# Kernel optimization log

Measured on AMD Instinct MI355X. Metric: run time of the kernel, lower is better.

## Reference

```python
import jax, jax.numpy as jnp
import numpy as np

B, L, H, N = 8, 8192, 128, 32  # batch, seq_len, d_model, d_state//2 (complex)


def setup_inputs() -> dict:
    key = jax.random.key(0)
    ks = jax.random.split(key, 13)
    x = jax.random.normal(ks[0], (B, L, 2), dtype=jnp.float32)
    enc_w = jax.random.normal(ks[1], (2, H), dtype=jnp.float32) * (1.0 / np.sqrt(2.0))
    enc_b = jax.random.normal(ks[2], (H,), dtype=jnp.float32) * 0.01
    # S4D init: dt log-uniform in [1e-3, 1e-1], A = -0.5 + i*pi*n (S4D-Lin)
    u01 = jax.random.uniform(ks[3], (H,), dtype=jnp.float32)
    log_dt = u01 * (np.log(0.1) - np.log(0.001)) + np.log(0.001)
    log_A_real = jnp.full((H, N), np.log(0.5), dtype=jnp.float32)
    A_imag = jnp.broadcast_to(np.pi * jnp.arange(N, dtype=jnp.float32), (H, N)).copy()
    C_re = jax.random.normal(ks[4], (H, N), dtype=jnp.float32) * (0.5 ** 0.5)
    C_im = jax.random.normal(ks[5], (H, N), dtype=jnp.float32) * (0.5 ** 0.5)
    D = jax.random.normal(ks[6], (H,), dtype=jnp.float32)
    out_w = jax.random.normal(ks[7], (2 * H, H), dtype=jnp.float32) * (1.0 / np.sqrt(H))
    out_b = jax.random.normal(ks[8], (2 * H,), dtype=jnp.float32) * 0.01
    dec_w = jax.random.normal(ks[9], (H, 1), dtype=jnp.float32) * (1.0 / np.sqrt(H))
    dec_b = jax.random.normal(ks[10], (1,), dtype=jnp.float32) * 0.01
    return {"x": x, "enc_w": enc_w, "enc_b": enc_b, "log_dt": log_dt,
            "log_A_real": log_A_real, "A_imag": A_imag, "C_re": C_re,
            "C_im": C_im, "D": D, "out_w": out_w, "out_b": out_b,
            "dec_w": dec_w, "dec_b": dec_b}


def reference(x, enc_w, enc_b, log_dt, log_A_real, A_imag, C_re, C_im, D,
              out_w, out_b, dec_w, dec_b):
    # Encoder (B,L,2) -> (B,L,H), then transpose to channels-first (B,H,L)
    u = jnp.einsum('blc,ch->blh', x, enc_w) + enc_b
    u = jnp.swapaxes(u, -1, -2)  # (B,H,L)
    Lx = u.shape[-1]

    # --- S4D kernel (zero-order-hold discretization, diagonal A) ---
    dt = jnp.exp(log_dt)                      # (H,)
    A = -jnp.exp(log_A_real) + 1j * A_imag    # (H,N) complex
    C = C_re + 1j * C_im                      # (H,N)
    dtA = dt[:, None] * A                     # (H,N)
    K_coef = C * (jnp.exp(dtA) - 1.0) / A     # (H,N)
    # Vandermonde: exp(dtA * l), l = 0..L-1  -> (H,N,L)
    vand = jnp.exp(dtA[:, :, None] * jnp.arange(Lx, dtype=jnp.float32))
    K = 2.0 * jnp.einsum('hn,hnl->hl', K_coef, vand).real  # (H,L)

    # --- causal convolution via FFT (length 2L avoids circular wrap) ---
    n = 2 * Lx
    y = jnp.fft.irfft(jnp.fft.rfft(u, n) * jnp.fft.rfft(K, n), n)[..., :Lx]
    y = y + D[:, None] * u                    # skip connection

    # GELU -> pointwise GLU output projection (Conv1d(H, 2H, 1) + GLU)
    y = jax.nn.gelu(y)
    z = jnp.einsum('bhl,gh->bgl', y, out_w) + out_b[None, :, None]  # (B,2H,L)
    a, g = jnp.split(z, 2, axis=1)
    y = a * jax.nn.sigmoid(g)                 # (B,H,L)

    # Mean-pool over sequence, decode to scalar: (B,1)
    pooled = jnp.mean(y, axis=-1)             # (B,H)
    return pooled @ dec_w + dec_b
```

## Files before the change

### kernel.cpp

```cpp
#include <hip/hip_runtime.h>
#include <math.h>

#define B_ 8
#define L_ 8192
#define H_ 128
#define N_ 32
#define C_ 128
#define T_ 64


typedef _Float16 half8 __attribute__((ext_vector_type(8)));
typedef __attribute__((ext_vector_type(4))) float f32x4;

__device__ __forceinline__ float gelu_tanh(float y) {
    float t = 0.7978845608028654f * fmaf(0.044715f, y * y * y, y);
    float e = __expf(2.f * t);
    float th = 1.f - __fdividef(2.f, e + 1.f);
    return 0.5f * y * (1.f + th);
}
__device__ __forceinline__ unsigned short f2h(float f) {
    _Float16 h = (_Float16)f;
    return *(unsigned short*)&h;
}
__device__ __forceinline__ float h2f(unsigned short u) {
    return (float)(*(const _Float16*)&u);
}
__device__ __forceinline__ unsigned int pk2(float a, float b) {
    return (unsigned)f2h(a) | ((unsigned)f2h(b) << 16);
}

__global__ __launch_bounds__(256, 4) void k_s4d(
    const float* __restrict__ x, const float* __restrict__ enc_w,
    const float* __restrict__ enc_b, const float* __restrict__ log_dt,
    const float* __restrict__ log_A_real, const float* __restrict__ A_imag,
    const float* __restrict__ C_re, const float* __restrict__ C_im,
    const float* __restrict__ Dp, const float* __restrict__ out_w,
    unsigned short* __restrict__ Wh, unsigned short* __restrict__ gy)
{
    const int bh = blockIdx.x;
    const int b = bh >> 7, h = bh & (H_ - 1);
    const int tid = threadIdx.x;
    const int lane = tid & 63, wq = tid >> 6;
    const int mrow = lane & 15, quad = lane >> 4;

    __shared__ unsigned short Ut[C_][72];
    __shared__ __align__(16) char scratch[18432];
    __shared__ float2 wTpow[7][N_];
    __shared__ float2 coefs[N_];
    __shared__ float2 ArAi[N_];
    __shared__ float  Kd[64];
    unsigned short* E16 = (unsigned short*)scratch;
    float2*         Sx  = (float2*)scratch;
    unsigned short* St  = (unsigned short*)scratch;

    const float dt = expf(log_dt[h]);
    const float Dh = Dp[h];

    if (tid < N_) {
        int n = tid;
        float Ar = -expf(log_A_real[h * N_ + n]);
        float Ai = A_imag[h * N_ + n];
        ArAi[n] = make_float2(Ar, Ai);
        float ar = dt * Ar, ai = dt * Ai;
        float er = expf(ar);
        float wr = er * cosf(ai), wi = er * sinf(ai);
        float inv = 1.f / (Ar * Ar + Ai * Ai);
        float numr = wr - 1.f, numi = wi;
        float qr = (numr * Ar + numi * Ai) * inv;
        float qi = (numi * Ar - numr * Ai) * inv;
        coefs[n] = make_float2(C_re[h * N_ + n] * qr - C_im[h * N_ + n] * qi,
                               C_re[h * N_ + n] * qi + C_im[h * N_ + n] * qr);
        float arT = dt * Ar * (float)T_, aiT = dt * Ai * (float)T_;
        float erT = expf(arT);
        float pr = erT * cosf(aiT), pi = erT * sinf(aiT);
#pragma unroll
        for (int k = 0; k < 7; ++k) {
            wTpow[k][n] = make_float2(pr, pi);
            float nr = pr * pr - pi * pi;
            pi = 2.f * pr * pi; pr = nr;
        }
    }

    if (b == 0) {
        int g = 2 * h + (tid >> 7), j = tid & 127;
        Wh[g * 128 + j] = f2h(out_w[g * 128 + j]);
    }

    const float ew0 = enc_w[h], ew1 = enc_w[H_ + h], eb = enc_b[h];
    {
        int c = tid >> 1, j0 = (tid & 1) * 32;
        const float4* xp = (const float4*)((const float2*)x + (size_t)b * L_
                                           + c * 64 + j0);
#pragma unroll
        for (int i = 0; i < 16; ++i) {
            float4 xv = xp[i];
            float u0 = fmaf(xv.x, ew0, fmaf(xv.y, ew1, eb));
            float u1 = fmaf(xv.z, ew0, fmaf(xv.w, ew1, eb));
            *(unsigned int*)&Ut[c][j0 + 2 * i] = pk2(u0, u1);
        }
    }
    __syncthreads();

    {
        int t = tid >> 2, q = tid & 3;
        float s = 0.f;
        float ft = (float)t;
#pragma unroll
        for (int k = 0; k < 8; ++k) {
            int n = q * 8 + k;
            float2 cf = coefs[n]; float2 aa = ArAi[n];
            float er = __expf(dt * aa.x * ft);
            float sn, cs; __sincosf(dt * aa.y * ft, &sn, &cs);
            s = fmaf(cf.x, er * cs, s);
            s = fmaf(-cf.y, er * sn, s);
        }
        ((float*)&Ut[t][64])[q] = s;
    }

    {
        f32x4 acc[8];
#pragma unroll
        for (int nt = 0; nt < 8; ++nt) acc[nt] = (f32x4){0.f, 0.f, 0.f, 0.f};
        const int m = wq * 16 + mrow;
        const float2 aa = ArAi[m & 31];
        const float dAr = dt * aa.x, dAi = dt * aa.y;
        const bool isIm = (m >= 32);
#pragma unroll
        for (int ks = 0; ks < 2; ++ks) {
            int k0 = ks * 32 + quad * 8;
            half8 af;
#pragma unroll
            for (int i = 0; i < 8; ++i) {
                float d = (float)(63 - (k0 + i));
                float er = __expf(dAr * d);
                float sn, cs; __sincosf(dAi * d, &sn, &cs);
                af[i] = (_Float16)(isIm ? er * sn : er * cs);
            }
#pragma unroll
            for (int nt = 0; nt < 8; ++nt) {
                half8 bf = *(const half8*)&Ut[nt * 16 + mrow][k0];
                acc[nt] = __builtin_amdgcn_mfma_f32_16x16x32_f16(
                    af, bf, acc[nt], 0, 0, 0);
            }
        }
        const int m0 = wq * 16 + quad * 4;
#pragma unroll
        for (int nt = 0; nt < 8; ++nt) {
            int cc = nt * 16 + mrow;
            unsigned long long w =
                (unsigned long long)pk2(acc[nt][0], acc[nt][1]) |
                ((unsigned long long)pk2(acc[nt][2], acc[nt][3]) << 32);
            *(unsigned long long*)&E16[cc * 72 + m0] = w;
        }
    }
    __syncthreads();

    if (tid < 64) {
        const float* kp = (const float*)&Ut[tid][64];
        Kd[tid] = 2.f * (kp[0] + kp[1] + kp[2] + kp[3])
                  + ((tid == 0) ? Dh : 0.f);
    }

    float zr[16], zi[16];
    const int cHalf = wq & 1, nHalf = wq >> 1;
    const int n0 = nHalf * 16;
    const int c = cHalf * 64 + lane;
    {
        half8 ha = *(const half8*)(E16 + c * 72 + n0);
        half8 hb = *(const half8*)(E16 + c * 72 + n0 + 8);
        half8 hc = *(const half8*)(E16 + c * 72 + 32 + n0);
        half8 hd = *(const half8*)(E16 + c * 72 + 32 + n0 + 8);
#pragma unroll
        for (int j = 0; j < 8; ++j) {
            zr[j] = (float)ha[j];  zr[8 + j] = (float)hb[j];
            zi[j] = (float)hc[j];  zi[8 + j] = (float)hd[j];
        }
    }
    __syncthreads();
#pragma unroll
    for (int k = 0; k < 6; ++k) {
        int s = 1 << k;
        float mask = (lane >= s) ? 1.f : 0.f;
#pragma unroll
        for (int j = 0; j < 16; ++j) {
            float2 q = wTpow[k][n0 + j];
            float vr = __shfl_up(zr[j], s, 64);
            float vi = __shfl_up(zi[j], s, 64);
            float adr = fmaf(q.x, vr, -(q.y * vi));
            float adi = fmaf(q.x, vi, q.y * vr);
            zr[j] = fmaf(mask, adr, zr[j]);
            zi[j] = fmaf(mask, adi, zi[j]);
        }
    }
    if (cHalf == 0) {
#pragma unroll
        for (int j = 0; j < 16; ++j)
            Sx[(n0 + j) * 64 + lane] = make_float2(zr[j], zi[j]);
    }
    __syncthreads();
    if (cHalf == 1) {
#pragma unroll
        for (int j = 0; j < 16; ++j) {
            float2 q = wTpow[6][n0 + j];
            float2 v = Sx[(n0 + j) * 64 + lane];
            zr[j] = fmaf(q.x, v.x, fmaf(-q.y, v.y, zr[j]));
            zi[j] = fmaf(q.x, v.y, fmaf(q.y, v.x, zi[j]));
        }
    }
    {
        bool l0 = (lane == 0);
#pragma unroll
        for (int j = 0; j < 16; ++j) {
            float2 bv = Sx[(n0 + j) * 64 + 63];
            float br = (cHalf == 1) ? bv.x : 0.f;
            float bi = (cHalf == 1) ? bv.y : 0.f;
            float tr = __shfl_up(zr[j], 1, 64);
            float ti = __shfl_up(zi[j], 1, 64);
            zr[j] = l0 ? br : tr;
            zi[j] = l0 ? bi : ti;
        }
    }
    __syncthreads();
    {
        uint4 w0, w1;
        w0.x = pk2(zr[0], zr[1]);   w0.y = pk2(zr[2], zr[3]);
        w0.z = pk2(zr[4], zr[5]);   w0.w = pk2(zr[6], zr[7]);
        w1.x = pk2(zr[8], zr[9]);   w1.y = pk2(zr[10], zr[11]);
        w1.z = pk2(zr[12], zr[13]); w1.w = pk2(zr[14], zr[15]);
        *(uint4*)&St[c * 72 + n0] = w0;
        *(uint4*)&St[c * 72 + n0 + 8] = w1;
        w0.x = pk2(zi[0], zi[1]);   w0.y = pk2(zi[2], zi[3]);
        w0.z = pk2(zi[4], zi[5]);   w0.w = pk2(zi[6], zi[7]);
        w1.x = pk2(zi[8], zi[9]);   w1.y = pk2(zi[10], zi[11]);
        w1.z = pk2(zi[12], zi[13]); w1.w = pk2(zi[14], zi[15]);
        *(uint4*)&St[c * 72 + 32 + n0] = w0;
        *(uint4*)&St[c * 72 + 32 + n0 + 8] = w1;
    }
    __syncthreads();

    {
        f32x4 acc[8];
#pragma unroll
        for (int nt = 0; nt < 8; ++nt) acc[nt] = (f32x4){0.f, 0.f, 0.f, 0.f};
        const int t = wq * 16 + mrow;
#pragma unroll
        for (int ks = 0; ks < 2; ++ks) {
            int k0 = ks * 32 + quad * 8;
            half8 af;
#pragma unroll
            for (int i = 0; i < 8; ++i) {
                int j = k0 + i;
                af[i] = (_Float16)((t >= j) ? Kd[t - j] : 0.f);
            }
#pragma unroll
            for (int nt = 0; nt < 8; ++nt) {
                half8 bf = *(const half8*)&Ut[nt * 16 + mrow][k0];
                acc[nt] = __builtin_amdgcn_mfma_f32_16x16x32_f16(
                    bf, af, acc[nt], 0, 0, 0);
            }
        }
        half8 afP0, afP1;
        {
            float tp1 = (float)(t + 1);
#pragma unroll
            for (int i = 0; i < 8; ++i) {
                int n = quad * 8 + i;
                float2 cf = coefs[n]; float2 aa = ArAi[n];
                float er = __expf(dt * aa.x * tp1);
                float sn, cs; __sincosf(dt * aa.y * tp1, &sn, &cs);
                float wr = er * cs, wi = er * sn;
                afP0[i] = (_Float16)( 2.f * (cf.x * wr - cf.y * wi));
                afP1[i] = (_Float16)(-2.f * (cf.x * wi + cf.y * wr));
            }
        }
#pragma unroll
        for (int ks = 0; ks < 2; ++ks) {
            int k0 = ks * 32 + quad * 8;
            half8 af = ks ? afP1 : afP0;
#pragma unroll
            for (int nt = 0; nt < 8; ++nt) {
                half8 bf = *(const half8*)&St[(nt * 16 + mrow) * 72 + k0];
                acc[nt] = __builtin_amdgcn_mfma_f32_16x16x32_f16(
                    bf, af, acc[nt], 0, 0, 0);
            }
        }
        unsigned short* gyr = gy + (size_t)bh * L_ + (size_t)t * 128;
#pragma unroll
        for (int nt = 0; nt < 8; ++nt) {
            float g0 = gelu_tanh(acc[nt][0]);
            float g1 = gelu_tanh(acc[nt][1]);
            float g2 = gelu_tanh(acc[nt][2]);
            float g3 = gelu_tanh(acc[nt][3]);
            unsigned long long w =
                (unsigned long long)pk2(g0, g1) |
                ((unsigned long long)pk2(g2, g3) << 32);
            *(unsigned long long*)&gyr[nt * 16 + quad * 4] = w;
        }
    }
}

__global__ __launch_bounds__(256, 4) void k_mix(
    const unsigned short* __restrict__ Wh, const unsigned short* __restrict__ gy,
    const float* __restrict__ out_b, const float* __restrict__ dec_w,
    float* __restrict__ part)
{
    __shared__ unsigned short Bt[64 * 128];
    __shared__ float red[4];

    const int blk = blockIdx.x;
    const int b = blk >> 7;
    const int t = (blk >> 1) & 63, ch = blk & 1;
    const int tid = threadIdx.x;
    const int wq = tid >> 6, lane = tid & 63;

    const unsigned short* gsrc = gy + (size_t)(b * H_) * L_ + t * 128 + ch * 64;
#pragma unroll
    for (int it = 0; it < 4; ++it) {
        int idx = it * 256 + tid;
        int h = idx >> 3, v0 = (idx & 7) * 8;
        uint4 q = *(const uint4*)(gsrc + (size_t)h * L_ + v0);
        const int sw = (((h >> 3) ^ (idx & 7)) << 3) | (h & 7);
        Bt[(v0 + 0) * 128 + sw] = (unsigned short)(q.x & 0xFFFF);
        Bt[(v0 + 1) * 128 + sw] = (unsigned short)(q.x >> 16);
        Bt[(v0 + 2) * 128 + sw] = (unsigned short)(q.y & 0xFFFF);
        Bt[(v0 + 3) * 128 + sw] = (unsigned short)(q.y >> 16);
        Bt[(v0 + 4) * 128 + sw] = (unsigned short)(q.z & 0xFFFF);
        Bt[(v0 + 5) * 128 + sw] = (unsigned short)(q.z >> 16);
        Bt[(v0 + 6) * 128 + sw] = (unsigned short)(q.w & 0xFFFF);
        Bt[(v0 + 7) * 128 + sw] = (unsigned short)(q.w >> 16);
    }
    __syncthreads();

    const int ga = wq * 32;
    const int gg = 128 + wq * 32;
    const int mrow = lane & 15;
    const int quad = lane >> 4;
    f32x4 accA[2][4], accG[2][4];
#pragma unroll
    for (int mt = 0; mt < 2; ++mt)
#pragma unroll
        for (int nt = 0; nt < 4; ++nt) {
            accA[mt][nt] = (f32x4){0.f, 0.f, 0.f, 0.f};
            accG[mt][nt] = (f32x4){0.f, 0.f, 0.f, 0.f};
        }

#pragma unroll
    for (int k = 0; k < 4; ++k) {
        const int h0 = k * 32 + quad * 8;
        half8 bfr[4];
#pragma unroll
        for (int nt = 0; nt < 4; ++nt) {
            int v = nt * 16 + mrow;
            bfr[nt] = *(const half8*)&Bt[v * 128 +
                                         (((4 * k + quad) ^ (v >> 3)) << 3)];
        }
#pragma unroll
        for (int mt = 0; mt < 2; ++mt) {
            half8 ah = *(const half8*)(Wh + (ga + mt * 16 + mrow) * 128 + h0);
            half8 ag = *(const half8*)(Wh + (gg + mt * 16 + mrow) * 128 + h0);
#pragma unroll
            for (int nt = 0; nt < 4; ++nt) {
                accA[mt][nt] = __builtin_amdgcn_mfma_f32_16x16x32_f16(
                    ah, bfr[nt], accA[mt][nt], 0, 0, 0);
                accG[mt][nt] = __builtin_amdgcn_mfma_f32_16x16x32_f16(
                    ag, bfr[nt], accG[mt][nt], 0, 0, 0);
            }
        }
    }

    float s = 0.f;
#pragma unroll
    for (int mt = 0; mt < 2; ++mt) {
        float4 obA = *(const float4*)(out_b + ga + mt * 16 + quad * 4);
        float4 obG = *(const float4*)(out_b + gg + mt * 16 + quad * 4);
        float4 dv  = *(const float4*)(dec_w + ga + mt * 16 + quad * 4);
#pragma unroll
        for (int nt = 0; nt < 4; ++nt) {
#pragma unroll
            for (int r = 0; r < 4; ++r) {
                float a  = accA[mt][nt][r] + ((const float*)&obA)[r];
                float zg = accG[mt][nt][r] + ((const float*)&obG)[r];
                float sig = __fdividef(1.f, 1.f + __expf(-zg));
                s = fmaf(((const float*)&dv)[r], a * sig, s);
            }
        }
    }
#pragma unroll
    for (int off = 32; off; off >>= 1) s += __shfl_down(s, off, 64);
    if (lane == 0) red[wq] = s;
    __syncthreads();
    if (tid == 0) part[blk] = red[0] + red[1] + red[2] + red[3];
}

__global__ __launch_bounds__(512) void k_final(
    const float* __restrict__ part, const float* __restrict__ dec_b,
    float* __restrict__ out)
{
    int tid = threadIdx.x;
    int b = tid >> 6, lane = tid & 63;
    float s = part[b * 128 + lane] + part[b * 128 + 64 + lane];
#pragma unroll
    for (int off = 32; off; off >>= 1) s += __shfl_down(s, off, 64);
    if (lane == 0) out[b] = fmaf(s, 1.0f / (float)L_, dec_b[0]);
}

extern "C" void kernel_launch(void* const* d_in, const int* in_sizes, int n_in,
                              void* d_out, int out_size, void* d_ws, size_t ws_size,
                              hipStream_t stream)
{
    const float* x         = (const float*)d_in[0];
    const float* enc_w     = (const float*)d_in[1];
    const float* enc_b     = (const float*)d_in[2];
    const float* log_dt    = (const float*)d_in[3];
    const float* log_A_real= (const float*)d_in[4];
    const float* A_imag    = (const float*)d_in[5];
    const float* C_re      = (const float*)d_in[6];
    const float* C_im      = (const float*)d_in[7];
    const float* Dp        = (const float*)d_in[8];
    const float* out_w     = (const float*)d_in[9];
    const float* out_b     = (const float*)d_in[10];
    const float* dec_w     = (const float*)d_in[11];
    const float* dec_b     = (const float*)d_in[12];
    float* out = (float*)d_out;

    char* ws = (char*)d_ws;
    unsigned short* Wh = (unsigned short*)(ws);
    unsigned short* gy = (unsigned short*)(ws + 3211264);
    float* part        = (float*)(ws + 19988480);

    k_s4d<<<B_ * H_, 256, 0, stream>>>(x, enc_w, enc_b, log_dt, log_A_real,
                                       A_imag, C_re, C_im, Dp, out_w, Wh, gy);
    k_mix<<<B_ * 128, 256, 0, stream>>>(Wh, gy, out_b, dec_w, part);
    k_final<<<1, 512, 0, stream>>>(part, dec_b, out);
}
```

Measured before the change: 132.3 us.

## Fuse three kernels into one cooperative kernel with grid-wide syncs

Merges the S4D, mixing and final-reduction kernels into a single cooperative launch that uses grid syncs between phases, falling back to the three separate launches if the cooperative launch fails. The goal is to remove launch overhead and the gaps between kernels. In exchange, 1024 blocks must all be co-resident, and the grid syncs add cost. The fused kernel's shared-memory and register footprint may also limit occupancy in the mixing phase.

```diff
diff --git a/kernel.cpp b/kernel.cpp
--- a/kernel.cpp
+++ b/kernel.cpp
@@ -1,5 +1,8 @@
 #include <hip/hip_runtime.h>
+#include <hip/hip_cooperative_groups.h>
 #include <math.h>
+
+namespace cg = cooperative_groups;
 
 #define B_ 8
 #define L_ 8192
@@ -29,26 +32,21 @@
     return (unsigned)f2h(a) | ((unsigned)f2h(b) << 16);
 }
 
-__global__ __launch_bounds__(256, 4) void k_s4d(
+__device__ __forceinline__ void phaseA(
+    unsigned short (*Ut)[72], char* scratch, float2 (*wTpow)[N_],
+    float2* coefs, float2* ArAi, float* Kd,
     const float* __restrict__ x, const float* __restrict__ enc_w,
     const float* __restrict__ enc_b, const float* __restrict__ log_dt,
     const float* __restrict__ log_A_real, const float* __restrict__ A_imag,
     const float* __restrict__ C_re, const float* __restrict__ C_im,
     const float* __restrict__ Dp, const float* __restrict__ out_w,
-    unsigned short* __restrict__ Wh, unsigned short* __restrict__ gy)
-{
-    const int bh = blockIdx.x;
+    unsigned short* __restrict__ Wh, unsigned short* __restrict__ gy,
+    int bh, int tid)
+{
     const int b = bh >> 7, h = bh & (H_ - 1);
-    const int tid = threadIdx.x;
     const int lane = tid & 63, wq = tid >> 6;
     const int mrow = lane & 15, quad = lane >> 4;
 
-    __shared__ unsigned short Ut[C_][72];
-    __shared__ __align__(16) char scratch[18432];
-    __shared__ float2 wTpow[7][N_];
-    __shared__ float2 coefs[N_];
-    __shared__ float2 ArAi[N_];
-    __shared__ float  Kd[64];
     unsigned short* E16 = (unsigned short*)scratch;
     float2*         Sx  = (float2*)scratch;
     unsigned short* St  = (unsigned short*)scratch;
@@ -299,18 +297,14 @@
     }
 }
 
-__global__ __launch_bounds__(256, 4) void k_mix(
+__device__ __forceinline__ void phaseB(
+    unsigned short* Bt, float* red,
     const unsigned short* __restrict__ Wh, const unsigned short* __restrict__ gy,
     const float* __restrict__ out_b, const float* __restrict__ dec_w,
-    float* __restrict__ part)
-{
-    __shared__ unsigned short Bt[64 * 128];
-    __shared__ float red[4];
-
-    const int blk = blockIdx.x;
+    float* __restrict__ part, int blk, int tid)
+{
     const int b = blk >> 7;
     const int t = (blk >> 1) & 63, ch = blk & 1;
-    const int tid = threadIdx.x;
     const int wq = tid >> 6, lane = tid & 63;
 
     const unsigned short* gsrc = gy + (size_t)(b * H_) * L_ + t * 128 + ch * 64;
@@ -392,16 +386,84 @@
     if (tid == 0) part[blk] = red[0] + red[1] + red[2] + red[3];
 }
 
-__global__ __launch_bounds__(512) void k_final(
+__device__ __forceinline__ void phaseC(
+    const float* __restrict__ part, const float* __restrict__ dec_b,
+    float* __restrict__ out, int tid)
+{
+    int b2 = tid >> 5, i = tid & 31;
+    float sum = 0.f;
+#pragma unroll
+    for (int k = 0; k < 4; ++k)
+        sum += part[b2 * 128 + i + 32 * k];
+#pragma unroll
+    for (int off = 16; off; off >>= 1) sum += __shfl_down(sum, off, 32);
+    if (i == 0) out[b2] = fmaf(sum, 1.0f / (float)L_, dec_b[0]);
+}
+
+__global__ __launch_bounds__(256, 4) void k_all(
+    const float* __restrict__ x, const float* __restrict__ enc_w,
+    const float* __restrict__ enc_b, const float* __restrict__ log_dt,
+    const float* __restrict__ log_A_real, const float* __restrict__ A_imag,
+    const float* __restrict__ C_re, const float* __restrict__ C_im,
+    const float* __restrict__ Dp, const float* __restrict__ out_w,
+    const float* __restrict__ out_b, const float* __restrict__ dec_w,
+    const float* __restrict__ dec_b,
+    unsigned short* __restrict__ Wh, unsigned short* __restrict__ gy,
+    float* __restrict__ part, float* __restrict__ out)
+{
+    __shared__ unsigned short Ut[C_][72];
+    __shared__ __align__(16) char scratch[18432];
+    __shared__ float2 wTpow[7][N_];
+    __shared__ float2 coefs[N_];
+    __shared__ float2 ArAi[N_];
+    __shared__ float  Kd[64];
+    __shared__ float  red[4];
+
+    const int tid = threadIdx.x;
+    phaseA(Ut, scratch, wTpow, coefs, ArAi, Kd,
+           x, enc_w, enc_b, log_dt, log_A_real, A_imag, C_re, C_im, Dp,
+           out_w, Wh, gy, blockIdx.x, tid);
+    cg::this_grid().sync();
+    phaseB((unsigned short*)scratch, red, Wh, gy, out_b, dec_w, part,
+           blockIdx.x, tid);
+    cg::this_grid().sync();
+    if (blockIdx.x == 0) phaseC(part, dec_b, out, tid);
+}
+
+__global__ __launch_bounds__(256, 4) void k_s4d(
+    const float* __restrict__ x, const float* __restrict__ enc_w,
+    const float* __restrict__ enc_b, const float* __restrict__ log_dt,
+    const float* __restrict__ log_A_real, const float* __restrict__ A_imag,
+    const float* __restrict__ C_re, const float* __restrict__ C_im,
+    const float* __restrict__ Dp, const float* __restrict__ out_w,
+    unsigned short* __restrict__ Wh, unsigned short* __restrict__ gy)
+{
+    __shared__ unsigned short Ut[C_][72];
+    __shared__ __align__(16) char scratch[18432];
+    __shared__ float2 wTpow[7][N_];
+    __shared__ float2 coefs[N_];
+    __shared__ float2 ArAi[N_];
+    __shared__ float  Kd[64];
+    phaseA(Ut, scratch, wTpow, coefs, ArAi, Kd,
+           x, enc_w, enc_b, log_dt, log_A_real, A_imag, C_re, C_im, Dp,
+           out_w, Wh, gy, blockIdx.x, threadIdx.x);
+}
+
+__global__ __launch_bounds__(256, 4) void k_mix(
+    const unsigned short* __restrict__ Wh, const unsigned short* __restrict__ gy,
+    const float* __restrict__ out_b, const float* __restrict__ dec_w,
+    float* __restrict__ part)
+{
+    __shared__ unsigned short Bt[64 * 128];
+    __shared__ float red[4];
+    phaseB(Bt, red, Wh, gy, out_b, dec_w, part, blockIdx.x, threadIdx.x);
+}
+
+__global__ __launch_bounds__(256) void k_final(
     const float* __restrict__ part, const float* __restrict__ dec_b,
     float* __restrict__ out)
 {
-    int tid = threadIdx.x;
-    int b = tid >> 6, lane = tid & 63;
-    float s = part[b * 128 + lane] + part[b * 128 + 64 + lane];
-#pragma unroll
-    for (int off = 32; off; off >>= 1) s += __shfl_down(s, off, 64);
-    if (lane == 0) out[b] = fmaf(s, 1.0f / (float)L_, dec_b[0]);
+    phaseC(part, dec_b, out, threadIdx.x);
 }
 
 extern "C" void kernel_launch(void* const* d_in, const int* in_sizes, int n_in,
@@ -428,8 +490,19 @@
     unsigned short* gy = (unsigned short*)(ws + 3211264);
     float* part        = (float*)(ws + 19988480);
 
-    k_s4d<<<B_ * H_, 256, 0, stream>>>(x, enc_w, enc_b, log_dt, log_A_real,
-                                       A_imag, C_re, C_im, Dp, out_w, Wh, gy);
-    k_mix<<<B_ * 128, 256, 0, stream>>>(Wh, gy, out_b, dec_w, part);
-    k_final<<<1, 512, 0, stream>>>(part, dec_b, out);
-}
+    void* args[] = {
+        (void*)&x, (void*)&enc_w, (void*)&enc_b, (void*)&log_dt,
+        (void*)&log_A_real, (void*)&A_imag, (void*)&C_re, (void*)&C_im,
+        (void*)&Dp, (void*)&out_w, (void*)&out_b, (void*)&dec_w,
+        (void*)&dec_b, (void*)&Wh, (void*)&gy, (void*)&part, (void*)&out };
+
+    hipError_t err = hipLaunchCooperativeKernel(
+        (const void*)k_all, dim3(B_ * H_), dim3(256), args, 0, stream);
+    if (err != hipSuccess) {
+        k_s4d<<<B_ * H_, 256, 0, stream>>>(x, enc_w, enc_b, log_dt,
+                                           log_A_real, A_imag, C_re, C_im,
+                                           Dp, out_w, Wh, gy);
+        k_mix<<<B_ * 128, 256, 0, stream>>>(Wh, gy, out_b, dec_w, part);
+        k_final<<<1, 256, 0, stream>>>(part, dec_b, out);
+    }
+}
```

Result: slower. 334.1 us (+152.6%).

## Restructure chunk-state scan to two chunks per lane, removing cross-wave LDS pass

Applied to the files above, without the earlier changes.

The inter-chunk state scan now gives each lane two adjacent chunks and each wave 8 state modes, instead of splitting chunks across two waves. A local combine of the chunk pair replaces the cross-wave fix-up through shared memory and removes two barriers. The goal is less LDS traffic and synchronization, plus half the shuffle work per lane. The encoder writes to shared memory are also widened to 16-byte stores. In exchange the scan has one more shuffle step, and the register layout and store pattern change.

```diff
diff --git a/kernel.cpp b/kernel.cpp
--- a/kernel.cpp
+++ b/kernel.cpp
@@ -50,7 +50,6 @@
     __shared__ float2 ArAi[N_];
     __shared__ float  Kd[64];
     unsigned short* E16 = (unsigned short*)scratch;
-    float2*         Sx  = (float2*)scratch;
     unsigned short* St  = (unsigned short*)scratch;
 
     const float dt = expf(log_dt[h]);
@@ -92,11 +91,17 @@
         const float4* xp = (const float4*)((const float2*)x + (size_t)b * L_
                                            + c * 64 + j0);
 #pragma unroll
-        for (int i = 0; i < 16; ++i) {
-            float4 xv = xp[i];
-            float u0 = fmaf(xv.x, ew0, fmaf(xv.y, ew1, eb));
-            float u1 = fmaf(xv.z, ew0, fmaf(xv.w, ew1, eb));
-            *(unsigned int*)&Ut[c][j0 + 2 * i] = pk2(u0, u1);
+        for (int ii = 0; ii < 4; ++ii) {
+            uint4 w;
+            unsigned int* pw = (unsigned int*)&w;
+#pragma unroll
+            for (int q2 = 0; q2 < 4; ++q2) {
+                float4 xv = xp[ii * 4 + q2];
+                float u0 = fmaf(xv.x, ew0, fmaf(xv.y, ew1, eb));
+                float u1 = fmaf(xv.z, ew0, fmaf(xv.w, ew1, eb));
+                pw[q2] = pk2(u0, u1);
+            }
+            *(uint4*)&Ut[c][j0 + ii * 8] = w;
         }
     }
     __syncthreads();
@@ -161,80 +166,72 @@
                   + ((tid == 0) ? Dh : 0.f);
     }
 
-    float zr[16], zi[16];
-    const int cHalf = wq & 1, nHalf = wq >> 1;
-    const int n0 = nHalf * 16;
-    const int c = cHalf * 64 + lane;
-    {
-        half8 ha = *(const half8*)(E16 + c * 72 + n0);
-        half8 hb = *(const half8*)(E16 + c * 72 + n0 + 8);
-        half8 hc = *(const half8*)(E16 + c * 72 + 32 + n0);
-        half8 hd = *(const half8*)(E16 + c * 72 + 32 + n0 + 8);
+    float z0r[8], z0i[8], z1r[8], z1i[8], hpr[8], hpi[8];
+    const int n0 = wq * 8;
+    const int c0 = 2 * lane;
+    {
+        half8 ar_ = *(const half8*)(E16 + c0 * 72 + n0);
+        half8 ai_ = *(const half8*)(E16 + c0 * 72 + 32 + n0);
+        half8 br_ = *(const half8*)(E16 + (c0 + 1) * 72 + n0);
+        half8 bi_ = *(const half8*)(E16 + (c0 + 1) * 72 + 32 + n0);
 #pragma unroll
         for (int j = 0; j < 8; ++j) {
-            zr[j] = (float)ha[j];  zr[8 + j] = (float)hb[j];
-            zi[j] = (float)hc[j];  zi[8 + j] = (float)hd[j];
-        }
-    }
-    __syncthreads();
-#pragma unroll
-    for (int k = 0; k < 6; ++k) {
-        int s = 1 << k;
+            z0r[j] = (float)ar_[j];  z0i[j] = (float)ai_[j];
+            z1r[j] = (float)br_[j];  z1i[j] = (float)bi_[j];
+        }
+    }
+    __syncthreads();
+#pragma unroll
+    for (int j = 0; j < 8; ++j) {
+        float2 q = wTpow[0][n0 + j];
+        z1r[j] = fmaf(q.x, z0r[j], fmaf(-q.y, z0i[j], z1r[j]));
+        z1i[j] = fmaf(q.x, z0i[j], fmaf(q.y, z0r[j], z1i[j]));
+    }
+#pragma unroll
+    for (int k = 1; k <= 6; ++k) {
+        int s = 1 << (k - 1);
         float mask = (lane >= s) ? 1.f : 0.f;
 #pragma unroll
-        for (int j = 0; j < 16; ++j) {
+        for (int j = 0; j < 8; ++j) {
             float2 q = wTpow[k][n0 + j];
-            float vr = __shfl_up(zr[j], s, 64);
-            float vi = __shfl_up(zi[j], s, 64);
+            float vr = __shfl_up(z1r[j], s, 64);
+            float vi = __shfl_up(z1i[j], s, 64);
             float adr = fmaf(q.x, vr, -(q.y * vi));
             float adi = fmaf(q.x, vi, q.y * vr);
-            zr[j] = fmaf(mask, adr, zr[j]);
-            zi[j] = fmaf(mask, adi, zi[j]);
-        }
-    }
-    if (cHalf == 0) {
-#pragma unroll
-        for (int j = 0; j < 16; ++j)
-            Sx[(n0 + j) * 64 + lane] = make_float2(zr[j], zi[j]);
-    }
-    __syncthreads();
-    if (cHalf == 1) {
-#pragma unroll
-        for (int j = 0; j < 16; ++j) {
-            float2 q = wTpow[6][n0 + j];
-            float2 v = Sx[(n0 + j) * 64 + lane];
-            zr[j] = fmaf(q.x, v.x, fmaf(-q.y, v.y, zr[j]));
-            zi[j] = fmaf(q.x, v.y, fmaf(q.y, v.x, zi[j]));
+            z1r[j] = fmaf(mask, adr, z1r[j]);
+            z1i[j] = fmaf(mask, adi, z1i[j]);
         }
     }
     {
         bool l0 = (lane == 0);
 #pragma unroll
-        for (int j = 0; j < 16; ++j) {
-            float2 bv = Sx[(n0 + j) * 64 + 63];
-            float br = (cHalf == 1) ? bv.x : 0.f;
-            float bi = (cHalf == 1) ? bv.y : 0.f;
-            float tr = __shfl_up(zr[j], 1, 64);
-            float ti = __shfl_up(zi[j], 1, 64);
-            zr[j] = l0 ? br : tr;
-            zi[j] = l0 ? bi : ti;
-        }
-    }
-    __syncthreads();
-    {
-        uint4 w0, w1;
-        w0.x = pk2(zr[0], zr[1]);   w0.y = pk2(zr[2], zr[3]);
-        w0.z = pk2(zr[4], zr[5]);   w0.w = pk2(zr[6], zr[7]);
-        w1.x = pk2(zr[8], zr[9]);   w1.y = pk2(zr[10], zr[11]);
-        w1.z = pk2(zr[12], zr[13]); w1.w = pk2(zr[14], zr[15]);
-        *(uint4*)&St[c * 72 + n0] = w0;
-        *(uint4*)&St[c * 72 + n0 + 8] = w1;
-        w0.x = pk2(zi[0], zi[1]);   w0.y = pk2(zi[2], zi[3]);
-        w0.z = pk2(zi[4], zi[5]);   w0.w = pk2(zi[6], zi[7]);
-        w1.x = pk2(zi[8], zi[9]);   w1.y = pk2(zi[10], zi[11]);
-        w1.z = pk2(zi[12], zi[13]); w1.w = pk2(zi[14], zi[15]);
-        *(uint4*)&St[c * 72 + 32 + n0] = w0;
-        *(uint4*)&St[c * 72 + 32 + n0 + 8] = w1;
+        for (int j = 0; j < 8; ++j) {
+            float tr = __shfl_up(z1r[j], 1, 64);
+            float ti = __shfl_up(z1i[j], 1, 64);
+            hpr[j] = l0 ? 0.f : tr;
+            hpi[j] = l0 ? 0.f : ti;
+        }
+    }
+#pragma unroll
+    for (int j = 0; j < 8; ++j) {
+        float2 q = wTpow[0][n0 + j];
+        z0r[j] = fmaf(q.x, hpr[j], fmaf(-q.y, hpi[j], z0r[j]));
+        z0i[j] = fmaf(q.x, hpi[j], fmaf(q.y, hpr[j], z0i[j]));
+    }
+    {
+        uint4 w;
+        w.x = pk2(hpr[0], hpr[1]); w.y = pk2(hpr[2], hpr[3]);
+        w.z = pk2(hpr[4], hpr[5]); w.w = pk2(hpr[6], hpr[7]);
+        *(uint4*)&St[c0 * 72 + n0] = w;
+        w.x = pk2(hpi[0], hpi[1]); w.y = pk2(hpi[2], hpi[3]);
+        w.z = pk2(hpi[4], hpi[5]); w.w = pk2(hpi[6], hpi[7]);
+        *(uint4*)&St[c0 * 72 + 32 + n0] = w;
+        w.x = pk2(z0r[0], z0r[1]); w.y = pk2(z0r[2], z0r[3]);
+        w.z = pk2(z0r[4], z0r[5]); w.w = pk2(z0r[6], z0r[7]);
+        *(uint4*)&St[(c0 + 1) * 72 + n0] = w;
+        w.x = pk2(z0i[0], z0i[1]); w.y = pk2(z0i[2], z0i[3]);
+        w.z = pk2(z0i[4], z0i[5]); w.w = pk2(z0i[6], z0i[7]);
+        *(uint4*)&St[(c0 + 1) * 72 + 32 + n0] = w;
     }
     __syncthreads();
 
```

New measurement: 126.4 us. -4.4%, faster.
